# Performance work log

Measured on AMD Instinct MI355X. Metric: run time of the kernel, lower is better.

The kernel has to match this reference:

```python
import jax, jax.numpy as jnp
import numpy as np

B, S, DIM = 128, 256, 512          # batch, grid tokens (16*16), input feature dim
D = 128                             # embedding_dim
K = 16384                           # num_embeddings
GH = GW = 16                        # grid size
EPS = 1e-12


def setup_inputs() -> dict:
    key = jax.random.key(0)
    ks = jax.random.split(key, 10)
    return {
        "input_data_first": jax.random.normal(ks[0], (B, S, DIM), jnp.float32),
        "input_data_last": jax.random.normal(ks[1], (B, S, DIM), jnp.float32),
        "random_vector": jax.random.normal(ks[2], (B * 64, D), jnp.float32),
        "codebooks": jax.random.normal(ks[3], (K, D), jnp.float32),
        "W_in": jax.random.normal(ks[4], (DIM, D), jnp.float32) / np.sqrt(DIM),
        "b_in": jnp.zeros((D,), jnp.float32),
        "conv_w": jax.random.normal(ks[5], (D, D, 3, 3), jnp.float32) / np.sqrt(D * 9),
        "conv_b": jnp.zeros((D,), jnp.float32),
        "W_out": jax.random.normal(ks[6], (D, DIM), jnp.float32) / np.sqrt(D),
        "b_out": jnp.zeros((DIM,), jnp.float32),
        "codebooks_used": jnp.zeros((K,), jnp.int32),
    }


def _encode(x, W_in, b_in, conv_w, conv_b):
    h = x @ W_in + b_in                                  # [B,S,D]
    h = jnp.transpose(h, (0, 2, 1)).reshape(B, D, GH, GW)  # [B,D,16,16]
    h = jax.lax.conv_general_dilated(
        h, conv_w, window_strides=(2, 2), padding=[(1, 1), (1, 1)],
        dimension_numbers=("NCHW", "OIHW", "NCHW"))
    h = h + conv_b[None, :, None, None]                  # [B,D,8,8]
    h = h.reshape(B, D, -1)                              # [B,D,64]
    h = jnp.transpose(h, (0, 2, 1)).reshape(-1, D)       # [B*64, D]
    return h


def reference(input_data_first, input_data_last, random_vector, codebooks,
              W_in, b_in, conv_w, conv_b, W_out, b_out, codebooks_used):
    e_first = _encode(input_data_first, W_in, b_in, conv_w, conv_b)
    e_last = _encode(input_data_last, W_in, b_in, conv_w, conv_b)
    x = e_last - e_first                                 # [N,D]

    # squared-distance to every codebook entry: [N,K]
    dists = (jnp.sum(x * x, axis=1, keepdims=True)
             - 2.0 * (x @ codebooks.T)
             + jnp.sum(codebooks * codebooks, axis=1)[None, :])
    min_indices = jnp.argmin(dists, axis=1)              # [N]
    hard_q = codebooks[min_indices]                      # [N,D]

    norm_res = jnp.sqrt(jnp.sum((x - hard_q) ** 2, axis=1, keepdims=True))
    norm_rnd = jnp.sqrt(jnp.sum(random_vector ** 2, axis=1, keepdims=True))
    vq_error = (norm_res / norm_rnd + EPS) * random_vector
    quantized = x + vq_error                             # [N,D]

    counts = jnp.zeros((K,), jnp.float32).at[min_indices].add(1.0)
    avg_probs = counts / x.shape[0]
    perplexity = jnp.exp(-jnp.sum(avg_probs * jnp.log(avg_probs + EPS)))

    new_used = codebooks_used + counts.astype(jnp.int32)

    # decode (faithful to torch: raw memory reinterpretation, not inverse transpose)
    q = quantized.reshape(B, D, -1)                      # [B,D,64]
    q = jnp.transpose(q, (0, 2, 1))                      # [B,64,D]
    out = q @ W_out + b_out                              # [B,64,DIM]
    return out, perplexity, new_used, min_indices.reshape(B, -1)
```

## Files before the change

### kernel.cpp

```cpp
#include <hip/hip_runtime.h>
#include <math.h>

#define NROWS 8192
#define KCB   16384

using frag_ab = __attribute__((ext_vector_type(8))) short;
using frag_cd = __attribute__((ext_vector_type(4))) float;
using f32x4   = __attribute__((ext_vector_type(4))) float;
using f64x4   = __attribute__((ext_vector_type(4))) double;

__device__ inline unsigned short f2bf(float f) {
    unsigned u = __float_as_uint(f);
    return (unsigned short)((u + 0x7FFFu + ((u >> 16) & 1u)) >> 16);
}

__device__ inline int mfma_f64_probe(int pm[4], int pn[4], int kq) {
    f64x4 z; z[0] = 0.0; z[1] = 0.0; z[2] = 0.0; z[3] = 0.0;
    const double dl = (double)(threadIdx.x & 63);
    f64x4 d1 = __builtin_amdgcn_mfma_f64_16x16x4f64(dl, 1.0, z, 0, 0, 0);
    f64x4 d2 = __builtin_amdgcn_mfma_f64_16x16x4f64(1.0, dl, z, 0, 0, 0);
    const double pk = (double)(1 << (4 * kq));
    f64x4 d3 = __builtin_amdgcn_mfma_f64_16x16x4f64(pk, dl, z, 0, 0, 0);
    int okl = 1;
    #pragma unroll
    for (int s = 0; s < 4; ++s) {
        double v1 = d1[s] - 96.0, v2 = d2[s] - 96.0;
        int i1 = (int)v1, i2 = (int)v2;
        okl &= (d1[s] == (double)(96 + i1)) & (i1 >= 0) & (i1 < 64) & ((i1 & 3) == 0);
        okl &= (d2[s] == (double)(96 + i2)) & (i2 >= 0) & (i2 < 64) & ((i2 & 3) == 0);
        pm[s] = i1 >> 2;
        pn[s] = i2 >> 2;
        okl &= (d3[s] == 4369.0 * (double)pn[s] + 205056.0);
    }
    return __all(okl);
}

__global__ __launch_bounds__(256) void k_wt(const float* __restrict__ cw,
                                            float* __restrict__ W2) {
    int gid = blockIdx.x * 256 + threadIdx.x;
    if (gid >= 147456) return;
    int co = gid & 127;
    int ci = (gid >> 7) & 127;
    int kk = gid >> 14;
    W2[gid] = cw[(size_t)co * 1152 + ci * 9 + kk];
}

__global__ __launch_bounds__(256) void k_c2(const float* __restrict__ cb,
                                            float* __restrict__ c2f) {
    int k = blockIdx.x * 256 + threadIdx.x;
    const float* row = cb + (size_t)k * 128;
    double s = 0.0;
    #pragma unroll
    for (int d = 0; d < 128; d += 4) {
        float4 v = *(const float4*)(row + d);
        s += (double)v.x * v.x + (double)v.y * v.y
           + (double)v.z * v.z + (double)v.w * v.w;
    }
    c2f[k] = (float)s + 1024.0f;
}

__global__ __launch_bounds__(256) void k_cbbf(const float* __restrict__ cb,
                                              unsigned short* __restrict__ Cbb) {
    int gid = blockIdx.x * 256 + threadIdx.x;
    float4 v = ((const float4*)cb)[gid];
    ushort4 o;
    o.x = f2bf(v.x); o.y = f2bf(v.y); o.z = f2bf(v.z); o.w = f2bf(v.w);
    ((ushort4*)Cbb)[gid] = o;
}

__global__ __launch_bounds__(256) void k_encode_gemm(
    const float* __restrict__ last, const float* __restrict__ first,
    const float* __restrict__ W_in, double* __restrict__ H)
{
    __shared__ double As[32][66];
    __shared__ double Bs[32][132];
    const int tid  = threadIdx.x;
    const int lane = tid & 63;
    const int w    = tid >> 6;
    const int row0 = blockIdx.x * 64;
    const int wm   = (w & 1) * 32;
    const int wn   = (w >> 1) * 64;
    const int lm   = lane & 15;
    const int kq   = lane >> 4;

    int pm[4], pn[4];
    const int ok = mfma_f64_probe(pm, pn, kq);
    if (!ok) {
        #pragma unroll
        for (int s = 0; s < 4; ++s) { pm[s] = 4 * kq + s; pn[s] = lm; }
    }

    f64x4 acc[2][4];
    #pragma unroll
    for (int i = 0; i < 2; ++i)
        #pragma unroll
        for (int j = 0; j < 4; ++j)
            #pragma unroll
            for (int q = 0; q < 4; ++q) acc[i][j][q] = 0.0;

    const int ar = tid >> 2;
    const int ak = (tid & 3) * 8;
    const int bkk = tid >> 3;
    const int bc  = (tid & 7) * 16;

    for (int k0 = 0; k0 < 512; k0 += 32) {
        if (k0) __syncthreads();
        {
            const float* lp = last  + (size_t)(row0 + ar) * 512 + k0 + ak;
            const float* fp = first + (size_t)(row0 + ar) * 512 + k0 + ak;
            const float4 l0 = *(const float4*)(lp);
            const float4 l1 = *(const float4*)(lp + 4);
            const float4 f0 = *(const float4*)(fp);
            const float4 f1 = *(const float4*)(fp + 4);
            As[ak + 0][ar] = (double)l0.x - (double)f0.x;
            As[ak + 1][ar] = (double)l0.y - (double)f0.y;
            As[ak + 2][ar] = (double)l0.z - (double)f0.z;
            As[ak + 3][ar] = (double)l0.w - (double)f0.w;
            As[ak + 4][ar] = (double)l1.x - (double)f1.x;
            As[ak + 5][ar] = (double)l1.y - (double)f1.y;
            As[ak + 6][ar] = (double)l1.z - (double)f1.z;
            As[ak + 7][ar] = (double)l1.w - (double)f1.w;
        }
        {
            const float* wp = W_in + (size_t)(k0 + bkk) * 128 + bc;
            #pragma unroll
            for (int q = 0; q < 4; ++q) {
                const float4 b4 = *(const float4*)(wp + 4 * q);
                Bs[bkk][bc + 4 * q + 0] = (double)b4.x;
                Bs[bkk][bc + 4 * q + 1] = (double)b4.y;
                Bs[bkk][bc + 4 * q + 2] = (double)b4.z;
                Bs[bkk][bc + 4 * q + 3] = (double)b4.w;
            }
        }
        __syncthreads();
        if (ok) {
            #pragma unroll
            for (int kc = 0; kc < 8; ++kc) {
                const int kk = kc * 4 + kq;
                double a0 = As[kk][wm + lm];
                double a1 = As[kk][wm + 16 + lm];
                double b0 = Bs[kk][wn + lm];
                double b1 = Bs[kk][wn + 16 + lm];
                double b2 = Bs[kk][wn + 32 + lm];
                double b3 = Bs[kk][wn + 48 + lm];
                acc[0][0] = __builtin_amdgcn_mfma_f64_16x16x4f64(a0, b0, acc[0][0], 0, 0, 0);
                acc[0][1] = __builtin_amdgcn_mfma_f64_16x16x4f64(a0, b1, acc[0][1], 0, 0, 0);
                acc[0][2] = __builtin_amdgcn_mfma_f64_16x16x4f64(a0, b2, acc[0][2], 0, 0, 0);
                acc[0][3] = __builtin_amdgcn_mfma_f64_16x16x4f64(a0, b3, acc[0][3], 0, 0, 0);
                acc[1][0] = __builtin_amdgcn_mfma_f64_16x16x4f64(a1, b0, acc[1][0], 0, 0, 0);
                acc[1][1] = __builtin_amdgcn_mfma_f64_16x16x4f64(a1, b1, acc[1][1], 0, 0, 0);
                acc[1][2] = __builtin_amdgcn_mfma_f64_16x16x4f64(a1, b2, acc[1][2], 0, 0, 0);
                acc[1][3] = __builtin_amdgcn_mfma_f64_16x16x4f64(a1, b3, acc[1][3], 0, 0, 0);
            }
        } else {
            #pragma unroll 4
            for (int k = 0; k < 32; ++k) {
                double b0 = Bs[k][wn + lm];
                double b1 = Bs[k][wn + 16 + lm];
                double b2 = Bs[k][wn + 32 + lm];
                double b3 = Bs[k][wn + 48 + lm];
                #pragma unroll
                for (int i = 0; i < 2; ++i) {
                    const double* ap = &As[k][wm + i * 16 + 4 * kq];
                    #pragma unroll
                    for (int s = 0; s < 4; ++s) {
                        double a = ap[s];
                        acc[i][0][s] = fma(a, b0, acc[i][0][s]);
                        acc[i][1][s] = fma(a, b1, acc[i][1][s]);
                        acc[i][2][s] = fma(a, b2, acc[i][2][s]);
                        acc[i][3][s] = fma(a, b3, acc[i][3][s]);
                    }
                }
            }
        }
    }
    #pragma unroll
    for (int i = 0; i < 2; ++i)
        #pragma unroll
        for (int j = 0; j < 4; ++j)
            #pragma unroll
            for (int s = 0; s < 4; ++s)
                H[(size_t)(row0 + wm + i * 16 + pm[s]) * 128 + wn + j * 16 + pn[s]]
                    = acc[i][j][s];
}

__global__ __launch_bounds__(256) void k_conv(
    const double* __restrict__ H, const float* __restrict__ W2,
    double* __restrict__ X, unsigned short* __restrict__ Xb)
{
    __shared__ double Hs[5 * 2048];
    const int tid  = threadIdx.x;
    const int lane = tid & 63;
    const int w    = tid >> 6;
    const int n0   = blockIdx.x * 16;
    const int b    = blockIdx.x >> 2;
    const int j    = blockIdx.x & 3;
    const int ihbase = 4 * j - 1;
    const int wn   = w * 32;
    const int lm   = lane & 15;
    const int kq   = lane >> 4;

    int pm[4], pn[4];
    const int ok = mfma_f64_probe(pm, pn, kq);

    #pragma unroll
    for (int it = 0; it < 20; ++it) {
        int slot = it * 256 + tid;
        int r = slot >> 10;
        int rem = (slot & 1023) * 2;
        int ih = ihbase + r;
        double2 v = (ih >= 0)
            ? *(const double2*)(H + (size_t)b * 32768 + (size_t)ih * 2048 + rem)
            : make_double2(0.0, 0.0);
        *(double2*)&Hs[r * 2048 + rem] = v;
    }
    __syncthreads();

    if (ok) {
        f64x4 acc0, acc1;
        #pragma unroll
        for (int q = 0; q < 4; ++q) { acc0[q] = 0.0; acc1[q] = 0.0; }
        const int ow = lm & 7, ohl = lm >> 3;
        #pragma unroll
        for (int kh = 0; kh < 3; ++kh) {
            #pragma unroll
            for (int kw = 0; kw < 3; ++kw) {
                const int tap = kh * 3 + kw;
                const int iw  = 2 * ow - 1 + kw;
                const int ihr = 2 * ohl + kh;
                const int valid = (iw >= 0) & (ihbase + ihr >= 0);
                const int aoff = valid ? (ihr * 2048 + iw * 128 + kq) : 0;
                const double msk = valid ? 1.0 : 0.0;
                const float* wbase = W2 + (size_t)(tap * 128 + kq) * 128 + wn + lm;
                #pragma unroll 4
                for (int ci0 = 0; ci0 < 128; ci0 += 4) {
                    double a  = Hs[aoff + ci0] * msk;
                    double b0 = (double)wbase[ci0 * 128];
                    double b1 = (double)wbase[ci0 * 128 + 16];
                    acc0 = __builtin_amdgcn_mfma_f64_16x16x4f64(a, b0, acc0, 0, 0, 0);
                    acc1 = __builtin_amdgcn_mfma_f64_16x16x4f64(a, b1, acc1, 0, 0, 0);
                }
            }
        }
        #pragma unroll
        for (int s = 0; s < 4; ++s) {
            size_t n = n0 + pm[s];
            int c0 = wn + pn[s];
            X [n * 128 + c0]      = acc0[s];
            Xb[n * 128 + c0]      = f2bf((float)acc0[s]);
            X [n * 128 + c0 + 16] = acc1[s];
            Xb[n * 128 + c0 + 16] = f2bf((float)acc1[s]);
        }
    } else {
        const int co   = wn + (lane & 31);
        const int half = lane >> 5;
        double facc[8];
        #pragma unroll
        for (int i = 0; i < 8; ++i) facc[i] = 0.0;
        for (int ci = 0; ci < 128; ++ci) {
            #pragma unroll
            for (int kh = 0; kh < 3; ++kh) {
                #pragma unroll
                for (int kw = 0; kw < 3; ++kw) {
                    double wv = (double)W2[(size_t)((kh * 3 + kw) * 128 + ci) * 128 + co];
                    #pragma unroll
                    for (int i = 0; i < 8; ++i) {
                        int m = half * 8 + i;
                        int iw = 2 * (m & 7) - 1 + kw;
                        int ihr = 2 * (m >> 3) + kh;
                        double hv = (iw >= 0 && ihbase + ihr >= 0)
                                  ? Hs[ihr * 2048 + iw * 128 + ci] : 0.0;
                        facc[i] = fma(hv, wv, facc[i]);
                    }
                }
            }
        }
        #pragma unroll
        for (int i = 0; i < 8; ++i) {
            size_t n = n0 + half * 8 + i;
            X [n * 128 + co] = facc[i];
            Xb[n * 128 + co] = f2bf((float)facc[i]);
        }
    }
}

__global__ __launch_bounds__(256) void k_dist_mfma(
    const unsigned short* __restrict__ Xb, const unsigned short* __restrict__ Cbb,
    const float* __restrict__ c2f, int* __restrict__ cand)
{
    __shared__ __align__(16) unsigned short Xs[128 * 128];
    __shared__ __align__(16) unsigned short Cs[128 * 128];
    const int tid   = threadIdx.x;
    const int row0  = blockIdx.x * 128;
    const int split = blockIdx.y;
    const int lane  = tid & 63;
    const int w     = tid >> 6;
    const int quad  = lane >> 4;
    const int lm    = lane & 15;
    const int cw    = (w & 1) * 64;
    const int rw    = (w >> 1) * 64;

    #pragma unroll
    for (int it = 0; it < 8; ++it) {
        int flat = it * 256 + tid;
        int r = flat >> 4, ch = flat & 15;
        *(uint4*)&Xs[r * 128 + (((ch ^ r) & 15) << 3) + (ch & 16 ? 0 : 0)] =
            *(const uint4*)(Xb + (size_t)(row0 + r) * 128 + ch * 8);
    }

    unsigned k1[4], k2[4];
    #pragma unroll
    for (int j = 0; j < 4; ++j) { k1[j] = 0xFFFFFFFFu; k2[j] = 0xFFFFFFFFu; }

    for (int chunk = 0; chunk < 16; ++chunk) {
        const int kb = split * 2048 + chunk * 128;
        if (chunk) __syncthreads();
        #pragma unroll
        for (int it = 0; it < 8; ++it) {
            int flat = it * 256 + tid;
            int r = flat >> 4, ch = flat & 15;
            *(uint4*)&Cs[r * 128 + ((ch ^ (r & 15)) << 3)] =
                *(const uint4*)(Cbb + (size_t)(kb + r) * 128 + ch * 8);
        }
        __syncthreads();

        frag_cd acc[4][4];
        #pragma unroll
        for (int i = 0; i < 4; ++i)
            #pragma unroll
            for (int j = 0; j < 4; ++j)
                #pragma unroll
                for (int r = 0; r < 4; ++r) acc[i][j][r] = 0.f;

        #pragma unroll
        for (int kk = 0; kk < 4; ++kk) {
            const int chs = ((kk * 4 + quad) ^ lm) << 3;
            frag_ab a[4], b[4];
            #pragma unroll
            for (int i = 0; i < 4; ++i)
                a[i] = *(const frag_ab*)&Cs[(cw + i * 16 + lm) * 128 + chs];
            #pragma unroll
            for (int j = 0; j < 4; ++j)
                b[j] = *(const frag_ab*)&Xs[(rw + j * 16 + lm) * 128 + chs];
            #pragma unroll
            for (int i = 0; i < 4; ++i)
                #pragma unroll
                for (int j = 0; j < 4; ++j)
                    acc[i][j] = __builtin_amdgcn_mfma_f32_16x16x32_bf16(
                        a[i], b[j], acc[i][j], 0, 0, 0);
        }

        const int ib = chunk * 128 + cw + quad * 4;
        #pragma unroll
        for (int i = 0; i < 4; ++i) {
            f32x4 c2v = *(const f32x4*)(c2f + kb + cw + i * 16 + quad * 4);
            #pragma unroll
            for (int j = 0; j < 4; ++j) {
                #pragma unroll
                for (int r = 0; r < 4; ++r) {
                    float u = fmaf(-2.f, acc[i][j][r], c2v[r]);
                    unsigned key = (__float_as_uint(u) & 0xFFFFF800u)
                                 | (unsigned)(ib + i * 16 + r);
                    unsigned nk1 = min(key, k1[j]);
                    k2[j] = min(max(key, k1[j]), k2[j]);
                    k1[j] = nk1;
                }
            }
        }
    }

    __syncthreads();
    uint2* kred = (uint2*)Cs;
    #pragma unroll
    for (int j = 0; j < 4; ++j)
        kred[(rw + j * 16 + lm) * 8 + (w & 1) * 4 + quad] = make_uint2(k1[j], k2[j]);
    __syncthreads();
    if (tid < 128) {
        unsigned b1 = 0xFFFFFFFFu, b2 = 0xFFFFFFFFu;
        for (int e = 0; e < 8; ++e) {
            uint2 kv = kred[tid * 8 + e];
            unsigned n1 = min(kv.x, b1); b2 = min(max(kv.x, b1), b2); b1 = n1;
            n1 = min(kv.y, b1);          b2 = min(max(kv.y, b1), b2); b1 = n1;
        }
        int base = split * 2048;
        int* o = cand + (size_t)(row0 + tid) * 16 + split * 2;
        o[0] = base + (int)(b1 & 0x7FFu);
        o[1] = base + (int)(b2 & 0x7FFu);
    }
}

__global__ __launch_bounds__(256) void k_refine(
    const double* __restrict__ X, const float* __restrict__ cb,
    const int* __restrict__ cand, const float* __restrict__ rnd,
    int* __restrict__ counts, float* __restrict__ quant,
    float* __restrict__ out_mi)
{
    const int wid  = threadIdx.x >> 6;
    const int lane = threadIdx.x & 63;
    const int row  = blockIdx.x * 4 + wid;
    const double x0 = X[(size_t)row * 128 + lane];
    const double x1 = X[(size_t)row * 128 + 64 + lane];
    double bestv = 1e300; int bestk = 0;
    for (int c = 0; c < 16; ++c) {
        int k = cand[(size_t)row * 16 + c] & (KCB - 1);
        double t0 = x0 - (double)cb[(size_t)k * 128 + lane];
        double t1 = x1 - (double)cb[(size_t)k * 128 + 64 + lane];
        double s = t0 * t0 + t1 * t1;
        #pragma unroll
        for (int off = 32; off > 0; off >>= 1) s += __shfl_xor(s, off, 64);
        if (s < bestv) { bestv = s; bestk = k; }
    }
    double r0 = (double)rnd[(size_t)row * 128 + lane];
    double r1 = (double)rnd[(size_t)row * 128 + 64 + lane];
    double rs = r0 * r0 + r1 * r1;
    #pragma unroll
    for (int off = 32; off > 0; off >>= 1) rs += __shfl_xor(rs, off, 64);
    double ratio = sqrt(bestv) / sqrt(rs) + 1e-12;
    quant[(size_t)row * 128 + lane]      = (float)(x0 + ratio * r0);
    quant[(size_t)row * 128 + 64 + lane] = (float)(x1 + ratio * r1);
    if (lane == 0) {
        out_mi[row] = (float)bestk;
        atomicAdd(counts + bestk, 1);
    }
}

__global__ __launch_bounds__(256) void k_perplex(
    const int* __restrict__ counts, const int* __restrict__ used_in,
    float* __restrict__ out_used, float* __restrict__ out_perp)
{
    __shared__ double red[256];
    int tid = threadIdx.x;
    double e = 0.0;
    for (int k = tid; k < KCB; k += 256) {
        int c = counts[k];
        out_used[k] = (float)(used_in[k] + c);
        if (c > 0) {
            double p = (double)c / 8192.0;
            e += p * log(p + 1e-12);
        }
    }
    red[tid] = e;
    __syncthreads();
    for (int s = 128; s > 0; s >>= 1) {
        if (tid < s) red[tid] += red[tid + s];
        __syncthreads();
    }
    if (tid == 0) out_perp[0] = (float)exp(-red[0]);
}

__global__ __launch_bounds__(256) void k_decode(
    const float* __restrict__ quant, const float* __restrict__ W_out,
    const float* __restrict__ b_out, float* __restrict__ out)
{
    __shared__ float As[8192];
    __shared__ float Bs[8192];
    const int tid = threadIdx.x;
    const int m0  = blockIdx.x * 64;
    const int b   = blockIdx.y;
    #pragma unroll
    for (int it = 0; it < 8; ++it) {
        int flat = it * 1024 + tid * 4;
        *(float4*)&As[flat] = *(const float4*)(quant + (size_t)b * 8192 + flat);
        int d2 = flat >> 6, m = flat & 63;
        *(float4*)&Bs[flat] = *(const float4*)(W_out + (size_t)d2 * 512 + m0 + m);
    }
    __syncthreads();
    const int tx = tid & 15, ty = tid >> 4;
    float acc[4][4];
    #pragma unroll
    for (int i = 0; i < 4; ++i)
        #pragma unroll
        for (int j = 0; j < 4; ++j) acc[i][j] = 0.f;
    #pragma unroll 8
    for (int d2 = 0; d2 < 128; ++d2) {
        float4 a  = *(const float4*)&As[d2 * 64 + ty * 4];
        float4 b4 = *(const float4*)&Bs[d2 * 64 + tx * 4];
        float av[4] = {a.x, a.y, a.z, a.w};
        float bv[4] = {b4.x, b4.y, b4.z, b4.w};
        #pragma unroll
        for (int i = 0; i < 4; ++i)
            #pragma unroll
            for (int j = 0; j < 4; ++j)
                acc[i][j] = fmaf(av[i], bv[j], acc[i][j]);
    }
    float4 bo = *(const float4*)(b_out + m0 + tx * 4);
    float bob[4] = {bo.x, bo.y, bo.z, bo.w};
    #pragma unroll
    for (int i = 0; i < 4; ++i) {
        int s2 = ty * 4 + i;
        float4 o;
        o.x = acc[i][0] + bob[0];
        o.y = acc[i][1] + bob[1];
        o.z = acc[i][2] + bob[2];
        o.w = acc[i][3] + bob[3];
        *(float4*)(out + (size_t)b * 32768 + (size_t)s2 * 512 + m0 + tx * 4) = o;
    }
}

extern "C" void kernel_launch(void* const* d_in, const int* in_sizes, int n_in,
                              void* d_out, int out_size, void* d_ws, size_t ws_size,
                              hipStream_t stream) {
    const float* first  = (const float*)d_in[0];
    const float* last   = (const float*)d_in[1];
    const float* rnd    = (const float*)d_in[2];
    const float* cb     = (const float*)d_in[3];
    const float* W_in   = (const float*)d_in[4];
    const float* conv_w = (const float*)d_in[6];
    const float* W_out  = (const float*)d_in[8];
    const float* b_out  = (const float*)d_in[9];
    const int*   used   = (const int*)d_in[10];

    float* out      = (float*)d_out;
    float* out_perp = out + 4194304;
    float* out_used = out + 4194305;
    float* out_mi   = out + 4194305 + 16384;

    char* ws = (char*)d_ws;
    double*         H      = (double*)(ws);
    double*         X      = (double*)(ws + 33554432);
    unsigned short* Cbb    = (unsigned short*)(ws + 41943040);
    float*          W2     = (float*) (ws + 46137344);
    float*          c2f    = (float*) (ws + 46727168);
    int*            cand   = (int*)   (ws + 46792704);
    float*          quant  = (float*) (ws + 47316992);
    int*            counts = (int*)   (ws + 51511296);
    unsigned short* Xb     = (unsigned short*)(ws + 51576832);

    hipMemsetAsync(counts, 0, KCB * sizeof(int), stream);
    k_wt<<<576, 256, 0, stream>>>(conv_w, W2);
    k_c2<<<64, 256, 0, stream>>>(cb, c2f);
    k_cbbf<<<2048, 256, 0, stream>>>(cb, Cbb);
    k_encode_gemm<<<512, 256, 0, stream>>>(last, first, W_in, H);
    k_conv<<<512, 256, 0, stream>>>(H, W2, X, Xb);
    k_dist_mfma<<<dim3(64, 8), 256, 0, stream>>>(Xb, Cbb, c2f, cand);
    k_refine<<<2048, 256, 0, stream>>>(X, cb, cand, rnd, counts, quant, out_mi);
    k_perplex<<<1, 256, 0, stream>>>(counts, used, out_used, out_perp);
    k_decode<<<dim3(8, 128), 256, 0, stream>>>(quant, W_out, b_out, out);
}
```

Measured before the change: 456.5 us.

## Shrink encode GEMM tile to 32 rows and read W_in directly from global

The encode GEMM block tile is halved from 64 to 32 rows and the K step doubled to 64, launching twice as many blocks. The shared-memory staging of W_in is removed: each lane now loads its B operand straight from global memory (L2/L1-resident) inside the MFMA loop, converting to double on the fly. This cuts LDS use and a sync-bounded copy stage and aims for higher occupancy, with a launch bound of 4 blocks per unit. The cost is more global loads of W_in per MFMA and less reuse per block.

```diff
diff --git a/kernel.cpp b/kernel.cpp
--- a/kernel.cpp
+++ b/kernel.cpp
@@ -68,18 +68,16 @@
     ((ushort4*)Cbb)[gid] = o;
 }
 
-__global__ __launch_bounds__(256) void k_encode_gemm(
+__global__ __launch_bounds__(256, 4) void k_encode_gemm(
     const float* __restrict__ last, const float* __restrict__ first,
     const float* __restrict__ W_in, double* __restrict__ H)
 {
-    __shared__ double As[32][66];
-    __shared__ double Bs[32][132];
+    __shared__ double As[64][33];
     const int tid  = threadIdx.x;
     const int lane = tid & 63;
     const int w    = tid >> 6;
-    const int row0 = blockIdx.x * 64;
-    const int wm   = (w & 1) * 32;
-    const int wn   = (w >> 1) * 64;
+    const int row0 = blockIdx.x * 32;
+    const int wn   = w * 32;
     const int lm   = lane & 15;
     const int kq   = lane >> 4;
 
@@ -90,85 +88,63 @@
         for (int s = 0; s < 4; ++s) { pm[s] = 4 * kq + s; pn[s] = lm; }
     }
 
-    f64x4 acc[2][4];
+    f64x4 acc[2][2];
     #pragma unroll
     for (int i = 0; i < 2; ++i)
         #pragma unroll
-        for (int j = 0; j < 4; ++j)
+        for (int j = 0; j < 2; ++j)
             #pragma unroll
             for (int q = 0; q < 4; ++q) acc[i][j][q] = 0.0;
 
-    const int ar = tid >> 2;
-    const int ak = (tid & 3) * 8;
-    const int bkk = tid >> 3;
-    const int bc  = (tid & 7) * 16;
-
-    for (int k0 = 0; k0 < 512; k0 += 32) {
+    const int srow = tid >> 3;
+    const int skb  = (tid & 7) * 8;
+
+    for (int k0 = 0; k0 < 512; k0 += 64) {
         if (k0) __syncthreads();
         {
-            const float* lp = last  + (size_t)(row0 + ar) * 512 + k0 + ak;
-            const float* fp = first + (size_t)(row0 + ar) * 512 + k0 + ak;
+            const float* lp = last  + (size_t)(row0 + srow) * 512 + k0 + skb;
+            const float* fp = first + (size_t)(row0 + srow) * 512 + k0 + skb;
             const float4 l0 = *(const float4*)(lp);
             const float4 l1 = *(const float4*)(lp + 4);
             const float4 f0 = *(const float4*)(fp);
             const float4 f1 = *(const float4*)(fp + 4);
-            As[ak + 0][ar] = (double)l0.x - (double)f0.x;
-            As[ak + 1][ar] = (double)l0.y - (double)f0.y;
-            As[ak + 2][ar] = (double)l0.z - (double)f0.z;
-            As[ak + 3][ar] = (double)l0.w - (double)f0.w;
-            As[ak + 4][ar] = (double)l1.x - (double)f1.x;
-            As[ak + 5][ar] = (double)l1.y - (double)f1.y;
-            As[ak + 6][ar] = (double)l1.z - (double)f1.z;
-            As[ak + 7][ar] = (double)l1.w - (double)f1.w;
-        }
-        {
-            const float* wp = W_in + (size_t)(k0 + bkk) * 128 + bc;
-            #pragma unroll
-            for (int q = 0; q < 4; ++q) {
-                const float4 b4 = *(const float4*)(wp + 4 * q);
-                Bs[bkk][bc + 4 * q + 0] = (double)b4.x;
-                Bs[bkk][bc + 4 * q + 1] = (double)b4.y;
-                Bs[bkk][bc + 4 * q + 2] = (double)b4.z;
-                Bs[bkk][bc + 4 * q + 3] = (double)b4.w;
-            }
+            As[skb + 0][srow] = (double)l0.x - (double)f0.x;
+            As[skb + 1][srow] = (double)l0.y - (double)f0.y;
+            As[skb + 2][srow] = (double)l0.z - (double)f0.z;
+            As[skb + 3][srow] = (double)l0.w - (double)f0.w;
+            As[skb + 4][srow] = (double)l1.x - (double)f1.x;
+            As[skb + 5][srow] = (double)l1.y - (double)f1.y;
+            As[skb + 6][srow] = (double)l1.z - (double)f1.z;
+            As[skb + 7][srow] = (double)l1.w - (double)f1.w;
         }
         __syncthreads();
         if (ok) {
             #pragma unroll
-            for (int kc = 0; kc < 8; ++kc) {
+            for (int kc = 0; kc < 16; ++kc) {
                 const int kk = kc * 4 + kq;
-                double a0 = As[kk][wm + lm];
-                double a1 = As[kk][wm + 16 + lm];
-                double b0 = Bs[kk][wn + lm];
-                double b1 = Bs[kk][wn + 16 + lm];
-                double b2 = Bs[kk][wn + 32 + lm];
-                double b3 = Bs[kk][wn + 48 + lm];
+                const float* wb = W_in + (size_t)(k0 + kk) * 128 + wn + lm;
+                double a0 = As[kk][lm];
+                double a1 = As[kk][16 + lm];
+                double b0 = (double)wb[0];
+                double b1 = (double)wb[16];
                 acc[0][0] = __builtin_amdgcn_mfma_f64_16x16x4f64(a0, b0, acc[0][0], 0, 0, 0);
                 acc[0][1] = __builtin_amdgcn_mfma_f64_16x16x4f64(a0, b1, acc[0][1], 0, 0, 0);
-                acc[0][2] = __builtin_amdgcn_mfma_f64_16x16x4f64(a0, b2, acc[0][2], 0, 0, 0);
-                acc[0][3] = __builtin_amdgcn_mfma_f64_16x16x4f64(a0, b3, acc[0][3], 0, 0, 0);
                 acc[1][0] = __builtin_amdgcn_mfma_f64_16x16x4f64(a1, b0, acc[1][0], 0, 0, 0);
                 acc[1][1] = __builtin_amdgcn_mfma_f64_16x16x4f64(a1, b1, acc[1][1], 0, 0, 0);
-                acc[1][2] = __builtin_amdgcn_mfma_f64_16x16x4f64(a1, b2, acc[1][2], 0, 0, 0);
-                acc[1][3] = __builtin_amdgcn_mfma_f64_16x16x4f64(a1, b3, acc[1][3], 0, 0, 0);
             }
         } else {
             #pragma unroll 4
-            for (int k = 0; k < 32; ++k) {
-                double b0 = Bs[k][wn + lm];
-                double b1 = Bs[k][wn + 16 + lm];
-                double b2 = Bs[k][wn + 32 + lm];
-                double b3 = Bs[k][wn + 48 + lm];
+            for (int k = 0; k < 64; ++k) {
+                double b0 = (double)W_in[(size_t)(k0 + k) * 128 + wn + lm];
+                double b1 = (double)W_in[(size_t)(k0 + k) * 128 + wn + 16 + lm];
                 #pragma unroll
                 for (int i = 0; i < 2; ++i) {
-                    const double* ap = &As[k][wm + i * 16 + 4 * kq];
+                    const double* ap = &As[k][16 * i + 4 * kq];
                     #pragma unroll
                     for (int s = 0; s < 4; ++s) {
                         double a = ap[s];
                         acc[i][0][s] = fma(a, b0, acc[i][0][s]);
                         acc[i][1][s] = fma(a, b1, acc[i][1][s]);
-                        acc[i][2][s] = fma(a, b2, acc[i][2][s]);
-                        acc[i][3][s] = fma(a, b3, acc[i][3][s]);
                     }
                 }
             }
@@ -177,10 +153,10 @@
     #pragma unroll
     for (int i = 0; i < 2; ++i)
         #pragma unroll
-        for (int j = 0; j < 4; ++j)
+        for (int j = 0; j < 2; ++j)
             #pragma unroll
             for (int s = 0; s < 4; ++s)
-                H[(size_t)(row0 + wm + i * 16 + pm[s]) * 128 + wn + j * 16 + pn[s]]
+                H[(size_t)(row0 + 16 * i + pm[s]) * 128 + wn + 16 * j + pn[s]]
                     = acc[i][j][s];
 }
 
@@ -530,7 +506,7 @@
     k_wt<<<576, 256, 0, stream>>>(conv_w, W2);
     k_c2<<<64, 256, 0, stream>>>(cb, c2f);
     k_cbbf<<<2048, 256, 0, stream>>>(cb, Cbb);
-    k_encode_gemm<<<512, 256, 0, stream>>>(last, first, W_in, H);
+    k_encode_gemm<<<1024, 256, 0, stream>>>(last, first, W_in, H);
     k_conv<<<512, 256, 0, stream>>>(H, W2, X, Xb);
     k_dist_mfma<<<dim3(64, 8), 256, 0, stream>>>(Xb, Cbb, c2f, cand);
     k_refine<<<2048, 256, 0, stream>>>(X, cb, cand, rnd, counts, quant, out_mi);
```

New measurement: 432.9 us. 5.2% less time.
